# Kernel tuning notes

Hardware: AMD Instinct MI355X
Metric: run time of the kernel (lower is better)

Reference implementation:

```python
import jax, jax.numpy as jnp
import numpy as np

D_MODEL = 2048
NUM_HEADS = 16
D_K = D_MODEL // NUM_HEADS


def setup_inputs() -> dict:
    key = jax.random.key(0)
    ks = jax.random.split(key, 9)
    s = 1.0 / np.sqrt(D_MODEL)
    x = jax.random.normal(ks[0], (4, 4096, D_MODEL), dtype=jnp.float32)
    wq = jax.random.uniform(ks[1], (D_MODEL, D_MODEL), jnp.float32, -s, s)
    bq = jax.random.uniform(ks[2], (D_MODEL,), jnp.float32, -s, s)
    wk = jax.random.uniform(ks[3], (D_MODEL, D_MODEL), jnp.float32, -s, s)
    bk = jax.random.uniform(ks[4], (D_MODEL,), jnp.float32, -s, s)
    wv = jax.random.uniform(ks[5], (D_MODEL, D_MODEL), jnp.float32, -s, s)
    bv = jax.random.uniform(ks[6], (D_MODEL,), jnp.float32, -s, s)
    wo = jax.random.uniform(ks[7], (D_MODEL, D_MODEL), jnp.float32, -s, s)
    bo = jax.random.uniform(ks[8], (D_MODEL,), jnp.float32, -s, s)
    return {"x": x, "wq": wq, "bq": bq, "wk": wk, "bk": bk,
            "wv": wv, "bv": bv, "wo": wo, "bo": bo}


def _heads(t, B, S):
    # (B, S, d_model) -> (B, H, S, d_k)
    return t.reshape(B, S, NUM_HEADS, D_K).transpose(0, 2, 1, 3)


def reference(x, wq, bq, wk, bk, wv, bv, wo, bo):
    B, S, _ = x.shape
    Q = _heads(x @ wq.T + bq, B, S)
    K = _heads(x @ wk.T + bk, B, S)
    V = _heads(x @ wv.T + bv, B, S)
    # elu(x)+1 feature map
    Q = jax.nn.elu(Q) + 1.0
    K = jax.nn.elu(K) + 1.0
    # KV: (B,H,d_k,d_k)
    KV = jnp.einsum('bhsd,bhse->bhde', K, V)
    QKV = jnp.einsum('bhsd,bhde->bhse', Q, KV)
    K_sum = jnp.sum(K, axis=-2)                      # (B,H,d_k)
    QK_sum = jnp.einsum('bhsd,bhd->bhs', Q, K_sum)   # (B,H,S)
    out = QKV / (QK_sum[..., None] + 1e-8)
    out = out.transpose(0, 2, 1, 3).reshape(B, S, D_MODEL)
    return out @ wo.T + bo
```

## Files before the change

kernel.cpp:

```cpp
#include <hip/hip_runtime.h>


#define D_MODEL 2048
#define SEQ     4096
#define BATCH   4
#define HEADS   16
#define DKH     128
#define M_TOK   16384
#define NBH     64

using frag8 = __attribute__((ext_vector_type(8))) short;
using f32x4 = __attribute__((ext_vector_type(4))) float;

typedef __attribute__((address_space(1))) const unsigned int g_u32;
typedef __attribute__((address_space(3))) unsigned int       l_u32;

__device__ __forceinline__ unsigned short f2bf(float f) {
  unsigned u = __float_as_uint(f);
  u = u + 0x7fffu + ((u >> 16) & 1u);
  return (unsigned short)(u >> 16);
}
__device__ __forceinline__ float bf2f(unsigned short h) {
  return __uint_as_float(((unsigned)h) << 16);
}

__global__ __launch_bounds__(256) void convert_all_kernel(
    const float* __restrict__ x,  const float* __restrict__ wq,
    const float* __restrict__ wk, const float* __restrict__ wv,
    const float* __restrict__ wo,
    unsigned short* __restrict__ xb,  unsigned short* __restrict__ wqb,
    unsigned short* __restrict__ wkb, unsigned short* __restrict__ wvb,
    unsigned short* __restrict__ wob) {
  const int bb = blockIdx.x;
  const float* in;
  unsigned short* out;
  long i;
  if (bb < 32768) {
    in = x; out = xb; i = (long)bb * 256 + threadIdx.x;
  } else {
    const int t = bb - 32768, s = t >> 12, r = t & 4095;
    i = (long)r * 256 + threadIdx.x;
    if (s == 0)      { in = wq; out = wqb; }
    else if (s == 1) { in = wk; out = wkb; }
    else if (s == 2) { in = wv; out = wvb; }
    else             { in = wo; out = wob; }
  }
  float4 v = reinterpret_cast<const float4*>(in)[i];
  ushort4 o;
  o.x = f2bf(v.x); o.y = f2bf(v.y); o.z = f2bf(v.z); o.w = f2bf(v.w);
  reinterpret_cast<ushort4*>(out)[i] = o;
}


#define ST_B(GB, LD, SLOT, KC)                                                \
  _Pragma("unroll") for (int j_ = 0; j_ < 2; ++j_)                            \
    __builtin_amdgcn_global_load_lds(                                         \
        (g_u32*)((GB) + (srow + wid * 16 + j_ * 8 + (lane >> 3)) * (LD)       \
                 + (KC) + scg * 8),                                           \
        (l_u32*)(sh + (SLOT) * 16384 + 8192 + (wid * 16 + j_ * 8) * 64),      \
        16, 0, 0);

#define ST_A(GA, LD, SP, ST, KC)                                              \
    __builtin_amdgcn_global_load_lds(                                         \
        (g_u32*)((GA) + (srow + (ST) * 32 + (wid & 3) * 8 + (lane >> 3)) * (LD) \
                 + (KC) + (wid >> 2) * 32 + scg * 8),                         \
        (l_u32*)(sh + ((SP) + (wid >> 2)) * 16384 +                           \
                 ((ST) * 32 + (wid & 3) * 8) * 64),                           \
        16, 0, 0);

#define RD_A(S0, S1, Q)                                                       \
  a0[0] = *(const frag8*)(lds + (S0) * 16384 + tA + (Q) * 2048);              \
  a0[1] = *(const frag8*)(lds + (S0) * 16384 + tA + (Q) * 2048 + 1024);       \
  a1[0] = *(const frag8*)(lds + (S1) * 16384 + tA + (Q) * 2048);              \
  a1[1] = *(const frag8*)(lds + (S1) * 16384 + tA + (Q) * 2048 + 1024);

#define RD_B(D0, D1, S0, S1)                                                  \
  _Pragma("unroll") for (int n_ = 0; n_ < 4; ++n_) {                          \
    D0[n_] = *(const frag8*)(lds + (S0) * 16384 + tB + n_ * 1024);            \
    D1[n_] = *(const frag8*)(lds + (S1) * 16384 + tB + n_ * 1024);            \
  }

#define MM8(AQ, B0, B1)                                                       \
  __builtin_amdgcn_s_setprio(1);                                              \
  _Pragma("unroll") for (int j_ = 0; j_ < 2; ++j_)                            \
  _Pragma("unroll") for (int n_ = 0; n_ < 4; ++n_)                            \
    acc[(AQ) + j_][n_] = __builtin_amdgcn_mfma_f32_16x16x32_bf16(             \
        a0[j_], B0[n_], acc[(AQ) + j_][n_], 0, 0, 0);                         \
  _Pragma("unroll") for (int j_ = 0; j_ < 2; ++j_)                            \
  _Pragma("unroll") for (int n_ = 0; n_ < 4; ++n_)                            \
    acc[(AQ) + j_][n_] = __builtin_amdgcn_mfma_f32_16x16x32_bf16(             \
        a1[j_], B1[n_], acc[(AQ) + j_][n_], 0, 0, 0);                         \
  __builtin_amdgcn_s_setprio(0);

#define BAR __builtin_amdgcn_s_barrier()
#define LG0                                                                   \
  asm volatile("s_waitcnt lgkmcnt(0)" ::: "memory");                          \
  __builtin_amdgcn_sched_barrier(0)

template <int MODE, bool XMAJOR>
__global__ __launch_bounds__(512, 2) void gemm256_nt_kernel(
    const unsigned short* __restrict__ A, long lda,
    const unsigned short* __restrict__ Bm, long ldb,
    void* __restrict__ Cv, long ldc,
    const float* __restrict__ bias, float* __restrict__ aux, int K) {
  __shared__ unsigned short sh[65536];
  const int lane = threadIdx.x & 63, wid = threadIdx.x >> 6;
  const int wm = wid >> 2, wn = wid & 3;
  const int lr = lane & 15, lh = lane >> 4;

  const int gx = gridDim.x, gy = gridDim.y;
  const int cpx = (gx * gy) >> 3;
  const int P = blockIdx.y * gx + blockIdx.x;
  const int Lw = (P & 7) * cpx + (P >> 3);
  int bx, by;
  if (XMAJOR) { bx = Lw / gy; by = Lw - bx * gy; }
  else        { by = Lw / gx; bx = Lw - by * gx; }

  const long m0 = (long)by * 256, n0 = (long)bx * 256;
  const unsigned short* Ablk = A + m0 * lda;
  const unsigned short* Bblk = Bm + n0 * ldb;
  const int NT = K >> 6;

  const int qA = (wm * 4 + lh) ^ (lr & 7);
  const int qB = ((wn >> 1) * 4 + lh) ^ (lr & 7);
  const unsigned short* lds = sh;
  const int tA = lr * 64 + qA * 8;
  const int tB = 8192 + ((wn & 1) * 64 + lr) * 64 + qB * 8;

  const int sqd = (lane & 7) ^ (lane >> 3);
  const int scg = sqd & 3;
  const long srow = (long)((sqd >> 2) * 128);

  f32x4 acc[8][4];
#pragma unroll
  for (int m = 0; m < 8; ++m)
#pragma unroll
    for (int n = 0; n < 4; ++n) acc[m][n] = (f32x4){0.f, 0.f, 0.f, 0.f};

  frag8 a0[2], a1[2], bu0[4], bu1[4], bv0[4], bv1[4];

  ST_B(Bblk, ldb, 0, 0)
  ST_B(Bblk, ldb, 1, 32)
  ST_A(Ablk, lda, 0, 0, 0) ST_A(Ablk, lda, 0, 1, 0)
  ST_A(Ablk, lda, 0, 2, 0) ST_A(Ablk, lda, 0, 3, 0)
  if (NT > 1) {
    ST_B(Bblk, ldb, 2, 64)
    ST_B(Bblk, ldb, 3, 96)
    ST_A(Ablk, lda, 2, 0, 64) ST_A(Ablk, lda, 2, 1, 64)
  }
  asm volatile("s_waitcnt vmcnt(6)" ::: "memory");
  BAR;

  const int NI = NT >> 1;
  for (int i = 0; i < NI; ++i) {
    const int kv = i * 128 + 64, kw = i * 128 + 128, kx = i * 128 + 192;
    const bool wok = (i + 1) < NI;
    RD_A(0, 1, 0)
    RD_B(bu0, bu1, 0, 1)
    ST_A(Ablk, lda, 2, 2, kv) ST_A(Ablk, lda, 2, 3, kv)
    asm volatile("s_waitcnt lgkmcnt(8)" ::: "memory");
    BAR; LG0;
    MM8(0, bu0, bu1)
    BAR;
    RD_A(0, 1, 1)
    if (wok) { ST_B(Bblk, ldb, 0, kw) }
    BAR; LG0;
    MM8(2, bu0, bu1)
    BAR;
    RD_A(0, 1, 2)
    if (wok) { ST_B(Bblk, ldb, 1, kw + 32) }
    BAR; LG0;
    MM8(4, bu0, bu1)
    BAR;
    RD_A(0, 1, 3)
    if (wok) { ST_A(Ablk, lda, 0, 0, kw) ST_A(Ablk, lda, 0, 1, kw) }
    if (wok) asm volatile("s_waitcnt vmcnt(6)" ::: "memory");
    else     asm volatile("s_waitcnt vmcnt(0)" ::: "memory");
    BAR; LG0;
    MM8(6, bu0, bu1)
    BAR;
    RD_A(2, 3, 0)
    RD_B(bv0, bv1, 2, 3)
    if (wok) { ST_A(Ablk, lda, 0, 2, kw) ST_A(Ablk, lda, 0, 3, kw) }
    asm volatile("s_waitcnt lgkmcnt(8)" ::: "memory");
    BAR; LG0;
    MM8(0, bv0, bv1)
    BAR;
    RD_A(2, 3, 1)
    if (wok) { ST_B(Bblk, ldb, 2, kx) }
    BAR; LG0;
    MM8(2, bv0, bv1)
    BAR;
    RD_A(2, 3, 2)
    if (wok) { ST_B(Bblk, ldb, 3, kx + 32) }
    BAR; LG0;
    MM8(4, bv0, bv1)
    BAR;
    RD_A(2, 3, 3)
    if (wok) { ST_A(Ablk, lda, 2, 0, kx) ST_A(Ablk, lda, 2, 1, kx)
               asm volatile("s_waitcnt vmcnt(6)" ::: "memory"); }
    BAR; LG0;
    MM8(6, bv0, bv1)
    BAR;
  }

  if constexpr (MODE == 1) {
    __shared__ float red2[256];
    if (threadIdx.x < 256) red2[threadIdx.x] = 0.f;
    __syncthreads();
#pragma unroll
    for (int m = 0; m < 8; ++m)
#pragma unroll
      for (int r = 0; r < 4; ++r) {
        const int lrow = wm * 128 + (m >> 1) * 32 + (m & 1) * 16 + lh * 4 + r;
        const long row = m0 + lrow;
        float part = 0.f;
#pragma unroll
        for (int n = 0; n < 4; ++n) {
          long col = n0 + wn * 64 + n * 16 + lr;
          float v = acc[m][n][r] + bias[row];
          v = v > 0.f ? v + 1.f : __expf(v);
          unsigned short us = f2bf(v);
          ((unsigned short*)Cv)[row * ldc + col] = us;
          part += bf2f(us);
        }
#pragma unroll
        for (int s = 1; s < 16; s <<= 1) part += __shfl_xor(part, s);
        if (lr == 0) atomicAdd(&red2[lrow], part);
      }
    __syncthreads();
    if (threadIdx.x < 256)
      atomicAdd(&aux[(n0 >> 12) * 2048 + m0 + threadIdx.x], red2[threadIdx.x]);
  } else {
#pragma unroll
    for (int m = 0; m < 8; ++m)
#pragma unroll
      for (int n = 0; n < 4; ++n)
#pragma unroll
        for (int r = 0; r < 4; ++r) {
          long row = m0 + wm * 128 + (m >> 1) * 32 + (m & 1) * 16 + lh * 4 + r;
          long col = n0 + wn * 64 + n * 16 + lr;
          float v = acc[m][n][r];
          if (MODE == 0) {
            v += bias[col]; v = v > 0.f ? v + 1.f : __expf(v);
            ((unsigned short*)Cv)[row * ldc + col] = f2bf(v);
          } else if (MODE == 2) {
            v += bias[row];
            ((unsigned short*)Cv)[row * ldc + col] = f2bf(v);
          } else {
            v += bias[col];
            ((float*)Cv)[row * ldc + col] = v;
          }
        }
  }
}

__device__ __forceinline__ void stage_tile(const unsigned short* __restrict__ G,
                                           long ld, unsigned short* __restrict__ L) {
  const int w = threadIdx.x >> 6, l = threadIdx.x & 63;
#pragma unroll
  for (int r = 0; r < 4; ++r) {
    const int chunk = w * 4 + r;
    const int row = chunk * 8 + (l >> 3);
    const int col = (l & 7) * 8;
    __builtin_amdgcn_global_load_lds((g_u32*)(G + (long)row * ld + col),
                                     (l_u32*)(L + chunk * 512), 16, 0, 0);
  }
}

__device__ __forceinline__ void gemm_mainloop(const unsigned short* __restrict__ A, long lda,
                                              const unsigned short* __restrict__ B, long ldb,
                                              int K, unsigned short* lA, unsigned short* lB,
                                              f32x4 acc[4][4]) {
  const int lane = threadIdx.x & 63;
  const int wid  = threadIdx.x >> 6;
  const int wr = wid >> 1, wc = wid & 1;
  const int lr = lane & 15, lh = lane >> 4;
  for (int k0 = 0; k0 < K; k0 += 64) {
    stage_tile(A + k0, lda, lA);
    stage_tile(B + k0, ldb, lB);
    __syncthreads();
#pragma unroll
    for (int kk = 0; kk < 64; kk += 32) {
      frag8 av[4], bv[4];
#pragma unroll
      for (int m = 0; m < 4; ++m)
        av[m] = *reinterpret_cast<const frag8*>(lA + (wr * 64 + m * 16 + lr) * 64 + kk + lh * 8);
#pragma unroll
      for (int n = 0; n < 4; ++n)
        bv[n] = *reinterpret_cast<const frag8*>(lB + (wc * 64 + n * 16 + lr) * 64 + kk + lh * 8);
#pragma unroll
      for (int m = 0; m < 4; ++m)
#pragma unroll
        for (int n = 0; n < 4; ++n)
          acc[m][n] = __builtin_amdgcn_mfma_f32_16x16x32_bf16(av[m], bv[n], acc[m][n], 0, 0, 0);
    }
    __syncthreads();
  }
}

#define ACC_INIT(acc)                                   \
  _Pragma("unroll") for (int m_ = 0; m_ < 4; ++m_)      \
  _Pragma("unroll") for (int n_ = 0; n_ < 4; ++n_)      \
      acc[m_][n_] = (f32x4){0.f, 0.f, 0.f, 0.f};

__global__ __launch_bounds__(256) void kvt_partial_kernel(
    const unsigned short* __restrict__ VT, const unsigned short* __restrict__ KT,
    float* __restrict__ part) {
  __shared__ unsigned short lA[128 * 64], lB[128 * 64];
  const int z = blockIdx.x;
  const int bh = z >> 3, c = z & 7;
  const int b = bh >> 4, h = bh & 15;
  const long tOff = (long)b * SEQ + (long)c * 512;
  const unsigned short* A  = VT + (long)(h * DKH) * M_TOK + tOff;
  const unsigned short* Bm = KT + (long)(h * DKH) * M_TOK + tOff;
  f32x4 acc[4][4];
  ACC_INIT(acc);
  gemm_mainloop(A, M_TOK, Bm, M_TOK, 512, lA, lB, acc);
  const int lane = threadIdx.x & 63, wid = threadIdx.x >> 6;
  const int wr = wid >> 1, wc = wid & 1, lr = lane & 15, lh = lane >> 4;
  float* out = part + (long)z * (DKH * DKH);
#pragma unroll
  for (int m = 0; m < 4; ++m)
#pragma unroll
    for (int n = 0; n < 4; ++n)
#pragma unroll
      for (int r = 0; r < 4; ++r) {
        int row = wr * 64 + m * 16 + lh * 4 + r;
        int col = wc * 64 + n * 16 + lr;
        out[row * DKH + col] = acc[m][n][r];
      }
}

__global__ __launch_bounds__(256) void reduce_kvt_kernel(
    const float* __restrict__ part, unsigned short* __restrict__ kvt) {
  int i = blockIdx.x * 256 + threadIdx.x;
  if (i < NBH * DKH * DKH) {
    int bh = i >> 14, j = i & 16383;
    float s = 0.f;
#pragma unroll
    for (int c = 0; c < 8; ++c) s += part[(((long)bh * 8 + c) << 14) + j];
    kvt[i] = f2bf(s);
  }
}

__global__ __launch_bounds__(256) void qkv_kernel(const unsigned short* __restrict__ Q,
                                                  const unsigned short* __restrict__ KVT,
                                                  const float* __restrict__ ksum,
                                                  unsigned short* __restrict__ attn) {
  __shared__ unsigned short lA[2][128 * 64], lB[2][128 * 64];
  __shared__ float qs[128];
  const int z = blockIdx.y, b = z >> 4, h = z & 15;
  const long mbase = (long)blockIdx.x * 512;
  const unsigned short* Bm = KVT + (long)z * (DKH * DKH);
  const float* ks = ksum + (long)b * 2048 + h * DKH;
  const int lane = threadIdx.x & 63, wid = threadIdx.x >> 6;
  const int wr = wid >> 1, wc = wid & 1, lr = lane & 15, lh = lane >> 4;
  const int qrow = threadIdx.x >> 1, qhalf = threadIdx.x & 1;

  stage_tile(Bm,      DKH, lB[0]);
  stage_tile(Bm + 64, DKH, lB[1]);

  for (int mt = 0; mt < 4; ++mt) {
    const unsigned short* A = Q + ((long)b * SEQ + mbase + mt * 128) * D_MODEL + h * DKH;
    stage_tile(A,      D_MODEL, lA[0]);
    stage_tile(A + 64, D_MODEL, lA[1]);
    __syncthreads();
    float qacc = 0.f;
    {
      const unsigned* pr = (const unsigned*)(lA[qhalf] + qrow * 64);
      const float* kk = ks + qhalf * 64;
#pragma unroll
      for (int j = 0; j < 32; ++j) {
        unsigned u = pr[j];
        qacc += bf2f((unsigned short)(u & 0xffff)) * kk[2 * j] +
                bf2f((unsigned short)(u >> 16)) * kk[2 * j + 1];
      }
    }
    qacc += __shfl_xor(qacc, 1);
    if (qhalf == 0) qs[qrow] = qacc;
    f32x4 acc[4][4];
    ACC_INIT(acc);
#pragma unroll
    for (int hf = 0; hf < 2; ++hf)
#pragma unroll
      for (int kk2 = 0; kk2 < 64; kk2 += 32) {
        frag8 av[4], bv[4];
#pragma unroll
        for (int m = 0; m < 4; ++m)
          av[m] = *reinterpret_cast<const frag8*>(lA[hf] + (wr * 64 + m * 16 + lr) * 64 + kk2 + lh * 8);
#pragma unroll
        for (int n = 0; n < 4; ++n)
          bv[n] = *reinterpret_cast<const frag8*>(lB[hf] + (wc * 64 + n * 16 + lr) * 64 + kk2 + lh * 8);
#pragma unroll
        for (int m = 0; m < 4; ++m)
#pragma unroll
          for (int n = 0; n < 4; ++n)
            acc[m][n] = __builtin_amdgcn_mfma_f32_16x16x32_bf16(av[m], bv[n], acc[m][n], 0, 0, 0);
      }
    __syncthreads();
#pragma unroll
    for (int m = 0; m < 4; ++m)
#pragma unroll
      for (int n = 0; n < 4; ++n)
#pragma unroll
        for (int r = 0; r < 4; ++r) {
          const int lrow = wr * 64 + m * 16 + lh * 4 + r;
          const long row = mbase + mt * 128 + lrow;
          const int col = wc * 64 + n * 16 + lr;
          float dnm = qs[lrow] + 1e-8f;
          float v = acc[m][n][r] / dnm;
          attn[((long)b * SEQ + row) * D_MODEL + h * DKH + col] = f2bf(v);
        }
  }
}

#define OFF_XB   0L
#define OFF_WQ   (OFF_XB + (long)M_TOK * D_MODEL * 2)
#define OFF_WK   (OFF_WQ + (long)D_MODEL * D_MODEL * 2)
#define OFF_WV   (OFF_WK + (long)D_MODEL * D_MODEL * 2)
#define OFF_WO   (OFF_WV + (long)D_MODEL * D_MODEL * 2)
#define OFF_QB   (OFF_WO + (long)D_MODEL * D_MODEL * 2)
#define OFF_KT   (OFF_QB + (long)M_TOK * D_MODEL * 2)
#define OFF_VT   (OFF_KT + (long)M_TOK * D_MODEL * 2)
#define OFF_PART (OFF_VT + (long)M_TOK * D_MODEL * 2)
#define OFF_KVT  (OFF_PART + (long)512 * DKH * DKH * 4)
#define OFF_KSUM (OFF_KVT + (long)NBH * DKH * DKH * 2)
#define OFF_QSUM (OFF_KSUM + (long)NBH * DKH * 4)
#define OFF_ATTN OFF_XB

extern "C" void kernel_launch(void* const* d_in, const int* in_sizes, int n_in,
                              void* d_out, int out_size, void* d_ws, size_t ws_size,
                              hipStream_t stream) {
  const float* x  = (const float*)d_in[0];
  const float* wq = (const float*)d_in[1];
  const float* bq = (const float*)d_in[2];
  const float* wk = (const float*)d_in[3];
  const float* bk = (const float*)d_in[4];
  const float* wv = (const float*)d_in[5];
  const float* bv = (const float*)d_in[6];
  const float* wo = (const float*)d_in[7];
  const float* bo = (const float*)d_in[8];

  char* ws = (char*)d_ws;
  unsigned short* xb   = (unsigned short*)(ws + OFF_XB);
  unsigned short* wqb  = (unsigned short*)(ws + OFF_WQ);
  unsigned short* wkb  = (unsigned short*)(ws + OFF_WK);
  unsigned short* wvb  = (unsigned short*)(ws + OFF_WV);
  unsigned short* wob  = (unsigned short*)(ws + OFF_WO);
  unsigned short* Qb   = (unsigned short*)(ws + OFF_QB);
  unsigned short* KTb  = (unsigned short*)(ws + OFF_KT);
  unsigned short* VTb  = (unsigned short*)(ws + OFF_VT);
  float*          part = (float*)(ws + OFF_PART);
  unsigned short* KVTb = (unsigned short*)(ws + OFF_KVT);
  float*          ksum = (float*)(ws + OFF_KSUM);
  unsigned short* attn = (unsigned short*)(ws + OFF_ATTN);

  dim3 blk(256);
  dim3 blk5(512);

  convert_all_kernel<<<49152, blk, 0, stream>>>(x, wq, wk, wv, wo,
                                                xb, wqb, wkb, wvb, wob);

  hipMemsetAsync(ksum, 0, NBH * DKH * sizeof(float), stream);

  gemm256_nt_kernel<0, false><<<dim3(D_MODEL / 256, M_TOK / 256), blk5, 0, stream>>>(
      xb, D_MODEL, wqb, D_MODEL, Qb, D_MODEL, bq, nullptr, D_MODEL);
  gemm256_nt_kernel<1, true><<<dim3(M_TOK / 256, D_MODEL / 256), blk5, 0, stream>>>(
      wkb, D_MODEL, xb, D_MODEL, KTb, M_TOK, bk, ksum, D_MODEL);
  gemm256_nt_kernel<2, true><<<dim3(M_TOK / 256, D_MODEL / 256), blk5, 0, stream>>>(
      wvb, D_MODEL, xb, D_MODEL, VTb, M_TOK, bv, nullptr, D_MODEL);

  kvt_partial_kernel<<<512, blk, 0, stream>>>(VTb, KTb, part);
  reduce_kvt_kernel<<<(NBH * DKH * DKH) / 256, blk, 0, stream>>>(part, KVTb);

  qkv_kernel<<<dim3(SEQ / 512, NBH), blk, 0, stream>>>(Qb, KVTb, ksum, attn);

  gemm256_nt_kernel<3, false><<<dim3(D_MODEL / 256, M_TOK / 256), blk5, 0, stream>>>(
      attn, D_MODEL, wob, D_MODEL, d_out, D_MODEL, bo, nullptr, D_MODEL);
}
```

Baseline: 653.3 us.

## Drop LDS waitcnt after barriers in GEMM loop; reduce KV partials via atomics

Removes the lgkmcnt(0) wait and sched_barrier that followed each barrier in the main 256-tile GEMM loop. This leans on the earlier lgkmcnt(8) waits and the compiler's own dependency waits to order LDS reads before the MFMAs, letting the compiler interleave them. Separately, the KV partial sums are now atomically added into one fp32 buffer that is zeroed beforehand, so the 8-way reduction kernel becomes a simple vectorized bf16 conversion. This adds atomic contention, and the missing explicit waits could risk ordering if the compiler does not insert them.

```diff
diff --git a/kernel.cpp b/kernel.cpp
--- a/kernel.cpp
+++ b/kernel.cpp
@@ -93,9 +93,6 @@
   __builtin_amdgcn_s_setprio(0);
 
 #define BAR __builtin_amdgcn_s_barrier()
-#define LG0                                                                   \
-  asm volatile("s_waitcnt lgkmcnt(0)" ::: "memory");                          \
-  __builtin_amdgcn_sched_barrier(0)
 
 template <int MODE, bool XMAJOR>
 __global__ __launch_bounds__(512, 2) void gemm256_nt_kernel(
@@ -159,47 +156,47 @@
     RD_B(bu0, bu1, 0, 1)
     ST_A(Ablk, lda, 2, 2, kv) ST_A(Ablk, lda, 2, 3, kv)
     asm volatile("s_waitcnt lgkmcnt(8)" ::: "memory");
-    BAR; LG0;
+    BAR;
     MM8(0, bu0, bu1)
     BAR;
     RD_A(0, 1, 1)
     if (wok) { ST_B(Bblk, ldb, 0, kw) }
-    BAR; LG0;
+    BAR;
     MM8(2, bu0, bu1)
     BAR;
     RD_A(0, 1, 2)
     if (wok) { ST_B(Bblk, ldb, 1, kw + 32) }
-    BAR; LG0;
+    BAR;
     MM8(4, bu0, bu1)
     BAR;
     RD_A(0, 1, 3)
     if (wok) { ST_A(Ablk, lda, 0, 0, kw) ST_A(Ablk, lda, 0, 1, kw) }
     if (wok) asm volatile("s_waitcnt vmcnt(6)" ::: "memory");
     else     asm volatile("s_waitcnt vmcnt(0)" ::: "memory");
-    BAR; LG0;
+    BAR;
     MM8(6, bu0, bu1)
     BAR;
     RD_A(2, 3, 0)
     RD_B(bv0, bv1, 2, 3)
     if (wok) { ST_A(Ablk, lda, 0, 2, kw) ST_A(Ablk, lda, 0, 3, kw) }
     asm volatile("s_waitcnt lgkmcnt(8)" ::: "memory");
-    BAR; LG0;
+    BAR;
     MM8(0, bv0, bv1)
     BAR;
     RD_A(2, 3, 1)
     if (wok) { ST_B(Bblk, ldb, 2, kx) }
-    BAR; LG0;
+    BAR;
     MM8(2, bv0, bv1)
     BAR;
     RD_A(2, 3, 2)
     if (wok) { ST_B(Bblk, ldb, 3, kx + 32) }
-    BAR; LG0;
+    BAR;
     MM8(4, bv0, bv1)
     BAR;
     RD_A(2, 3, 3)
     if (wok) { ST_A(Ablk, lda, 2, 0, kx) ST_A(Ablk, lda, 2, 1, kx)
                asm volatile("s_waitcnt vmcnt(6)" ::: "memory"); }
-    BAR; LG0;
+    BAR;
     MM8(6, bv0, bv1)
     BAR;
   }
@@ -306,7 +303,7 @@
 
 __global__ __launch_bounds__(256) void kvt_partial_kernel(
     const unsigned short* __restrict__ VT, const unsigned short* __restrict__ KT,
-    float* __restrict__ part) {
+    float* __restrict__ kvtf) {
   __shared__ unsigned short lA[128 * 64], lB[128 * 64];
   const int z = blockIdx.x;
   const int bh = z >> 3, c = z & 7;
@@ -319,7 +316,7 @@
   gemm_mainloop(A, M_TOK, Bm, M_TOK, 512, lA, lB, acc);
   const int lane = threadIdx.x & 63, wid = threadIdx.x >> 6;
   const int wr = wid >> 1, wc = wid & 1, lr = lane & 15, lh = lane >> 4;
-  float* out = part + (long)z * (DKH * DKH);
+  float* out = kvtf + (long)bh * (DKH * DKH);
 #pragma unroll
   for (int m = 0; m < 4; ++m)
 #pragma unroll
@@ -328,20 +325,17 @@
       for (int r = 0; r < 4; ++r) {
         int row = wr * 64 + m * 16 + lh * 4 + r;
         int col = wc * 64 + n * 16 + lr;
-        out[row * DKH + col] = acc[m][n][r];
+        atomicAdd(&out[row * DKH + col], acc[m][n][r]);
       }
 }
 
-__global__ __launch_bounds__(256) void reduce_kvt_kernel(
-    const float* __restrict__ part, unsigned short* __restrict__ kvt) {
+__global__ __launch_bounds__(256) void convert_kvt_kernel(
+    const float* __restrict__ kvtf, unsigned short* __restrict__ kvt) {
   int i = blockIdx.x * 256 + threadIdx.x;
-  if (i < NBH * DKH * DKH) {
-    int bh = i >> 14, j = i & 16383;
-    float s = 0.f;
-#pragma unroll
-    for (int c = 0; c < 8; ++c) s += part[(((long)bh * 8 + c) << 14) + j];
-    kvt[i] = f2bf(s);
-  }
+  float4 v = reinterpret_cast<const float4*>(kvtf)[i];
+  ushort4 o;
+  o.x = f2bf(v.x); o.y = f2bf(v.y); o.z = f2bf(v.z); o.w = f2bf(v.w);
+  reinterpret_cast<ushort4*>(kvt)[i] = o;
 }
 
 __global__ __launch_bounds__(256) void qkv_kernel(const unsigned short* __restrict__ Q,
@@ -423,10 +417,9 @@
 #define OFF_QB   (OFF_WO + (long)D_MODEL * D_MODEL * 2)
 #define OFF_KT   (OFF_QB + (long)M_TOK * D_MODEL * 2)
 #define OFF_VT   (OFF_KT + (long)M_TOK * D_MODEL * 2)
-#define OFF_PART (OFF_VT + (long)M_TOK * D_MODEL * 2)
-#define OFF_KVT  (OFF_PART + (long)512 * DKH * DKH * 4)
+#define OFF_KVTF (OFF_VT + (long)M_TOK * D_MODEL * 2)
+#define OFF_KVT  (OFF_KVTF + (long)NBH * DKH * DKH * 4)
 #define OFF_KSUM (OFF_KVT + (long)NBH * DKH * DKH * 2)
-#define OFF_QSUM (OFF_KSUM + (long)NBH * DKH * 4)
 #define OFF_ATTN OFF_XB
 
 extern "C" void kernel_launch(void* const* d_in, const int* in_sizes, int n_in,
@@ -451,7 +444,7 @@
   unsigned short* Qb   = (unsigned short*)(ws + OFF_QB);
   unsigned short* KTb  = (unsigned short*)(ws + OFF_KT);
   unsigned short* VTb  = (unsigned short*)(ws + OFF_VT);
-  float*          part = (float*)(ws + OFF_PART);
+  float*          kvtf = (float*)(ws + OFF_KVTF);
   unsigned short* KVTb = (unsigned short*)(ws + OFF_KVT);
   float*          ksum = (float*)(ws + OFF_KSUM);
   unsigned short* attn = (unsigned short*)(ws + OFF_ATTN);
@@ -463,6 +456,7 @@
                                                 xb, wqb, wkb, wvb, wob);
 
   hipMemsetAsync(ksum, 0, NBH * DKH * sizeof(float), stream);
+  hipMemsetAsync(kvtf, 0, (long)NBH * DKH * DKH * sizeof(float), stream);
 
   gemm256_nt_kernel<0, false><<<dim3(D_MODEL / 256, M_TOK / 256), blk5, 0, stream>>>(
       xb, D_MODEL, wqb, D_MODEL, Qb, D_MODEL, bq, nullptr, D_MODEL);
@@ -471,8 +465,8 @@
   gemm256_nt_kernel<2, true><<<dim3(M_TOK / 256, D_MODEL / 256), blk5, 0, stream>>>(
       wvb, D_MODEL, xb, D_MODEL, VTb, M_TOK, bv, nullptr, D_MODEL);
 
-  kvt_partial_kernel<<<512, blk, 0, stream>>>(VTb, KTb, part);
-  reduce_kvt_kernel<<<(NBH * DKH * DKH) / 256, blk, 0, stream>>>(part, KVTb);
+  kvt_partial_kernel<<<512, blk, 0, stream>>>(VTb, KTb, kvtf);
+  convert_kvt_kernel<<<(NBH * DKH * DKH / 4) / 256, blk, 0, stream>>>(kvtf, KVTb);
 
   qkv_kernel<<<dim3(SEQ / 512, NBH), blk, 0, stream>>>(Qb, KVTb, ksum, attn);
 
```

New measurement: 663.6 us. No clear change (+1.6%).
